# Optimization experiments

Hardware: AMD Instinct MI355X
Metric: run time of the kernel (lower is better)

Reference implementation:

```python
import jax, jax.numpy as jnp
import numpy as np

NUM_HEADS = 8


def setup_inputs() -> dict:
    key = jax.random.key(0)
    ks = jax.random.split(key, 10)
    B, S, E = 2, 2048, 1024
    return {
        "X": jax.random.normal(ks[0], (B, S, E), dtype=jnp.float32),
        "residual_score": jax.random.normal(ks[1], (S, S), dtype=jnp.float32) * 0.02,
        "Wq": jax.random.normal(ks[2], (E, E), dtype=jnp.float32) * 0.02,
        "Wk": jax.random.normal(ks[3], (E, E), dtype=jnp.float32) * 0.02,
        "Wv": jax.random.normal(ks[4], (E, E), dtype=jnp.float32) * 0.02,
        "Wepi": jax.random.normal(ks[5], (S, S), dtype=jnp.float32) * 0.02,
        "bq": jax.random.normal(ks[6], (S, 1), dtype=jnp.float32) * 0.02,
        "bk": jax.random.normal(ks[7], (S, 1), dtype=jnp.float32) * 0.02,
        "bv": jax.random.normal(ks[8], (S, 1), dtype=jnp.float32) * 0.02,
        "bo": jax.random.normal(ks[9], (S, 1), dtype=jnp.float32) * 0.02,
    }


def _split_heads(x, H):
    # (B, S, E) -> (B*H, S, E//H)
    B, S, E = x.shape
    return x.reshape(B, S, H, E // H).transpose(0, 2, 1, 3).reshape(B * H, S, E // H)


def _merge_heads(x, H):
    # (B*H, S, hd) -> (B, S, hd*H)
    BH, S, hd = x.shape
    B = BH // H
    return x.reshape(B, H, S, hd).transpose(0, 2, 1, 3).reshape(B, S, hd * H)


def reference(X, residual_score, Wq, Wk, Wv, Wepi, bq, bk, bv, bo):
    B, S, E = X.shape
    H = NUM_HEADS
    # QKV projections; biases are (S,1) broadcast over the feature axis
    q = X @ Wq + bq
    k = X @ Wk + bk
    v = X @ Wv + bv
    q = _split_heads(q, H)  # (B*H, S, hd)
    k = _split_heads(k, H)
    v = _split_heads(v, H)
    # NOTE: scaled by sqrt(seq_length), as in the original module
    attn = jnp.einsum('bsd,btd->bst', q, k) / jnp.sqrt(jnp.float32(S))
    attn = attn + residual_score  # (S,S) broadcasts over B*H
    score = jax.nn.softmax(attn, axis=-1) * Wepi  # learned elementwise mask
    effect = jnp.einsum('bst,btd->bsd', score, v)  # (B*H, S, hd)
    effect = _merge_heads(effect, H) + bo  # (B, S, E)
    return (effect, attn)
```

## Files before the change

kernel.cpp:

```cpp
#include <hip/hip_runtime.h>
#include <hip/hip_bf16.h>
#include <stdint.h>

#define S_LEN 2048
#define E_DIM 1024
#define NHEAD 8
#define HDIM 128
#define SCALE 0.022097086912079608f

typedef __attribute__((ext_vector_type(8))) short short8;
typedef __attribute__((ext_vector_type(4))) float f32x4;

__device__ __forceinline__ ushort f2bf(float f) {
  __hip_bfloat16 h = __float2bfloat16(f);
  return __builtin_bit_cast(ushort, h);
}

__device__ __forceinline__ void gload_lds16(const void* g, void* l) {
  __builtin_amdgcn_global_load_lds(
      (const __attribute__((address_space(1))) uint32_t*)g,
      (__attribute__((address_space(3))) uint32_t*)l, 16, 0, 0);
}

__global__ void cast_x_kernel(const float* __restrict__ X, ushort* __restrict__ Xb) {
  int i = (blockIdx.x * 256 + threadIdx.x) * 4;
  float4 v = *(const float4*)(X + i);
  ushort4 o;
  o.x = f2bf(v.x); o.y = f2bf(v.y); o.z = f2bf(v.z); o.w = f2bf(v.w);
  *(ushort4*)(Xb + i) = o;
}

__global__ void transpose_w_kernel(const float* __restrict__ W0, const float* __restrict__ W1,
                                   const float* __restrict__ W2, ushort* __restrict__ WT) {
  const float* W = blockIdx.z == 0 ? W0 : (blockIdx.z == 1 ? W1 : W2);
  ushort* out = WT + (size_t)blockIdx.z * E_DIM * E_DIM;
  int tk = blockIdx.x * 64, tn = blockIdx.y * 64;
  __shared__ float t[64][65];
  int tid = threadIdx.x;
  int rbase = tid >> 4;
  int cc4 = (tid & 15) * 4;
#pragma unroll
  for (int q = 0; q < 4; q++) {
    int row = q * 16 + rbase;
    float4 v = *(const float4*)(W + (size_t)(tk + row) * E_DIM + tn + cc4);
    t[row][cc4] = v.x; t[row][cc4 + 1] = v.y; t[row][cc4 + 2] = v.z; t[row][cc4 + 3] = v.w;
  }
  __syncthreads();
#pragma unroll
  for (int q = 0; q < 4; q++) {
    int row = q * 16 + rbase;
    ushort4 o;
    o.x = f2bf(t[cc4 + 0][row]);
    o.y = f2bf(t[cc4 + 1][row]);
    o.z = f2bf(t[cc4 + 2][row]);
    o.w = f2bf(t[cc4 + 3][row]);
    *(ushort4*)(out + (size_t)(tn + row) * E_DIM + tk + cc4) = o;
  }
}

__global__ __launch_bounds__(256)
void qkv_gemm_kernel(const ushort* __restrict__ Xb, const ushort* __restrict__ WT,
                     const float* __restrict__ bq, const float* __restrict__ bk,
                     const float* __restrict__ bv,
                     ushort* __restrict__ Qb, ushort* __restrict__ Kb, ushort* __restrict__ Vt) {
  int p = blockIdx.z;
  const ushort* Wp = WT + (size_t)p * E_DIM * E_DIM;
  const float* bias = (p == 0) ? bq : ((p == 1) ? bk : bv);
  int tm = blockIdx.x, tn = blockIdx.y;
  __shared__ ushort lA[128 * 64];
  __shared__ ushort lB[128 * 64];
  int tid = threadIdx.x, lane = tid & 63, w = tid >> 6;
  int wr = (w >> 1) * 64, wc = (w & 1) * 64;
  f32x4 acc[4][4] = {};
  const char* gA = (const char*)(Xb + (size_t)(tm * 128) * E_DIM);
  const char* gB = (const char*)(Wp + (size_t)(tn * 128) * E_DIM);
  char* sA = (char*)lA;
  char* sB = (char*)lB;
  for (int ks = 0; ks < E_DIM / 64; ks++) {
    int k0 = ks * 64;
#pragma unroll
    for (int rr = 0; rr < 4; rr++) {
      int c = rr * 256 + tid;
      int row = c >> 3, cc = c & 7;
      int sc = cc ^ (row & 7);
      size_t goff = ((size_t)row * E_DIM + k0 + sc * 8) * 2;
      int loff = (rr * 256 + (w << 6)) * 16;
      gload_lds16(gA + goff, sA + loff);
      gload_lds16(gB + goff, sB + loff);
    }
    __syncthreads();
#pragma unroll
    for (int kk = 0; kk < 2; kk++) {
      short8 af[4], bfr[4];
#pragma unroll
      for (int m = 0; m < 4; m++) {
        int row = wr + m * 16 + (lane & 15);
        int ch = (kk * 4 + (lane >> 4)) ^ (row & 7);
        af[m] = *(const short8*)(sA + row * 128 + ch * 16);
      }
#pragma unroll
      for (int n = 0; n < 4; n++) {
        int row = wc + n * 16 + (lane & 15);
        int ch = (kk * 4 + (lane >> 4)) ^ (row & 7);
        bfr[n] = *(const short8*)(sB + row * 128 + ch * 16);
      }
#pragma unroll
      for (int m = 0; m < 4; m++)
#pragma unroll
        for (int n = 0; n < 4; n++)
          acc[m][n] = __builtin_amdgcn_mfma_f32_16x16x32_bf16(af[m], bfr[n], acc[m][n], 0, 0, 0);
    }
    __syncthreads();
  }
#pragma unroll
  for (int m = 0; m < 4; m++) {
#pragma unroll
    for (int ri = 0; ri < 4; ri++) {
      int rg = tm * 128 + wr + m * 16 + (lane >> 4) * 4 + ri;
      float bsv = bias[rg & (S_LEN - 1)];
#pragma unroll
      for (int n = 0; n < 4; n++) {
        int cg = tn * 128 + wc + n * 16 + (lane & 15);
        ushort o = f2bf(acc[m][n][ri] + bsv);
        if (p == 0) {
          Qb[(size_t)rg * E_DIM + cg] = o;
        } else if (p == 1) {
          Kb[(size_t)rg * E_DIM + cg] = o;
        } else {
          int bb = rg >> 11, s2 = rg & (S_LEN - 1), hh = cg >> 7, dd = cg & (HDIM - 1);
          Vt[(((size_t)(bb * NHEAD + hh)) * HDIM + dd) * S_LEN + s2] = o;
        }
      }
    }
  }
}

__global__ __launch_bounds__(256)
void attn_gemm_kernel(const ushort* __restrict__ Qb, const ushort* __restrict__ Kb,
                      const float* __restrict__ resid, float* __restrict__ attn_out) {
  int tm = blockIdx.x, tn = blockIdx.y, bh = blockIdx.z;
  int b = bh >> 3, h = bh & 7;
  __shared__ ushort lA[128 * 64];
  __shared__ ushort lB[128 * 64];
  int tid = threadIdx.x, lane = tid & 63, w = tid >> 6;
  int wr = (w >> 1) * 64, wc = (w & 1) * 64;
  f32x4 acc[4][4] = {};
  const char* gA = (const char*)(Qb + ((size_t)(b * S_LEN + tm * 128)) * E_DIM + h * HDIM);
  const char* gB = (const char*)(Kb + ((size_t)(b * S_LEN + tn * 128)) * E_DIM + h * HDIM);
  char* sA = (char*)lA;
  char* sB = (char*)lB;
  for (int ks = 0; ks < 2; ks++) {
    int k0 = ks * 64;
#pragma unroll
    for (int rr = 0; rr < 4; rr++) {
      int c = rr * 256 + tid;
      int row = c >> 3, cc = c & 7;
      int sc = cc ^ (row & 7);
      size_t goff = ((size_t)row * E_DIM + k0 + sc * 8) * 2;
      int loff = (rr * 256 + (w << 6)) * 16;
      gload_lds16(gA + goff, sA + loff);
      gload_lds16(gB + goff, sB + loff);
    }
    __syncthreads();
#pragma unroll
    for (int kk = 0; kk < 2; kk++) {
      short8 af[4], bfr[4];
#pragma unroll
      for (int m = 0; m < 4; m++) {
        int row = wr + m * 16 + (lane & 15);
        int ch = (kk * 4 + (lane >> 4)) ^ (row & 7);
        af[m] = *(const short8*)(sA + row * 128 + ch * 16);
      }
#pragma unroll
      for (int n = 0; n < 4; n++) {
        int row = wc + n * 16 + (lane & 15);
        int ch = (kk * 4 + (lane >> 4)) ^ (row & 7);
        bfr[n] = *(const short8*)(sB + row * 128 + ch * 16);
      }
#pragma unroll
      for (int m = 0; m < 4; m++)
#pragma unroll
        for (int n = 0; n < 4; n++)
          acc[m][n] = __builtin_amdgcn_mfma_f32_16x16x32_bf16(af[m], bfr[n], acc[m][n], 0, 0, 0);
    }
    __syncthreads();
  }
  float* outp = attn_out + (size_t)bh * S_LEN * S_LEN;
#pragma unroll
  for (int m = 0; m < 4; m++) {
#pragma unroll
    for (int ri = 0; ri < 4; ri++) {
      int sg = tm * 128 + wr + m * 16 + (lane >> 4) * 4 + ri;
#pragma unroll
      for (int n = 0; n < 4; n++) {
        int tg = tn * 128 + wc + n * 16 + (lane & 15);
        outp[(size_t)sg * S_LEN + tg] = acc[m][n][ri] * SCALE + resid[(size_t)sg * S_LEN + tg];
      }
    }
  }
}

__global__ __launch_bounds__(256)
void pv_gemm_kernel(const float* __restrict__ attn, const float* __restrict__ Wepi,
                    const ushort* __restrict__ Vt, const float* __restrict__ bo,
                    float* __restrict__ effect) {
  int tm = blockIdx.x, bh = blockIdx.y;
  int b = bh >> 3, h = bh & 7;
  __shared__ ushort lA[128 * 64];
  __shared__ ushort lB[128 * 64];
  __shared__ float l_lds[256];
  int tid = threadIdx.x, lane = tid & 63, w = tid >> 6;
  int wr = (w >> 1) * 64, wc = (w & 1) * 64;
  f32x4 acc[4][4] = {};
  float lsum = 0.f;
  int r = tid >> 1, half = tid & 1;
  const float* aRow = attn + (size_t)bh * S_LEN * S_LEN + (size_t)(tm * 128 + r) * S_LEN + half * 32;
  const float* wRow = Wepi + (size_t)(tm * 128 + r) * S_LEN + half * 32;
  const char* gB = (const char*)(Vt + (size_t)bh * HDIM * S_LEN);
  char* sA = (char*)lA;
  char* sB = (char*)lB;
  for (int ks = 0; ks < S_LEN / 64; ks++) {
    int t0 = ks * 64;
#pragma unroll
    for (int rr = 0; rr < 4; rr++) {
      int c = rr * 256 + tid;
      int row = c >> 3, cc = c & 7;
      int sc = cc ^ (row & 7);
      gload_lds16(gB + ((size_t)row * S_LEN + t0 + sc * 8) * 2, sB + (rr * 256 + (w << 6)) * 16);
    }
#pragma unroll
    for (int cgrp = 0; cgrp < 4; cgrp++) {
      float4 a0 = *(const float4*)(aRow + t0 + cgrp * 8);
      float4 a1 = *(const float4*)(aRow + t0 + cgrp * 8 + 4);
      float4 w0 = *(const float4*)(wRow + t0 + cgrp * 8);
      float4 w1 = *(const float4*)(wRow + t0 + cgrp * 8 + 4);
      float e0 = __expf(a0.x), e1 = __expf(a0.y), e2 = __expf(a0.z), e3 = __expf(a0.w);
      float e4 = __expf(a1.x), e5 = __expf(a1.y), e6 = __expf(a1.z), e7 = __expf(a1.w);
      lsum += (e0 + e1 + e2 + e3) + (e4 + e5 + e6 + e7);
      short8 pk;
      pk[0] = (short)f2bf(e0 * w0.x); pk[1] = (short)f2bf(e1 * w0.y);
      pk[2] = (short)f2bf(e2 * w0.z); pk[3] = (short)f2bf(e3 * w0.w);
      pk[4] = (short)f2bf(e4 * w1.x); pk[5] = (short)f2bf(e5 * w1.y);
      pk[6] = (short)f2bf(e6 * w1.z); pk[7] = (short)f2bf(e7 * w1.w);
      int ch = (half * 4 + cgrp) ^ (r & 7);
      *(short8*)(sA + r * 128 + ch * 16) = pk;
    }
    __syncthreads();
#pragma unroll
    for (int kk = 0; kk < 2; kk++) {
      short8 af[4], bfr[4];
#pragma unroll
      for (int m = 0; m < 4; m++) {
        int row = wr + m * 16 + (lane & 15);
        int ch = (kk * 4 + (lane >> 4)) ^ (row & 7);
        af[m] = *(const short8*)(sA + row * 128 + ch * 16);
      }
#pragma unroll
      for (int n = 0; n < 4; n++) {
        int row = wc + n * 16 + (lane & 15);
        int ch = (kk * 4 + (lane >> 4)) ^ (row & 7);
        bfr[n] = *(const short8*)(sB + row * 128 + ch * 16);
      }
#pragma unroll
      for (int m = 0; m < 4; m++)
#pragma unroll
        for (int n = 0; n < 4; n++)
          acc[m][n] = __builtin_amdgcn_mfma_f32_16x16x32_bf16(af[m], bfr[n], acc[m][n], 0, 0, 0);
    }
    __syncthreads();
  }
  l_lds[tid] = lsum;
  __syncthreads();
#pragma unroll
  for (int m = 0; m < 4; m++) {
#pragma unroll
    for (int ri = 0; ri < 4; ri++) {
      int rl = wr + m * 16 + (lane >> 4) * 4 + ri;
      int sg = tm * 128 + rl;
      float linv = 1.0f / (l_lds[2 * rl] + l_lds[2 * rl + 1]);
      float bov = bo[sg];
#pragma unroll
      for (int n = 0; n < 4; n++) {
        int dg = wc + n * 16 + (lane & 15);
        effect[((size_t)(b * S_LEN + sg)) * E_DIM + h * HDIM + dg] = acc[m][n][ri] * linv + bov;
      }
    }
  }
}

extern "C" void kernel_launch(void* const* d_in, const int* in_sizes, int n_in,
                              void* d_out, int out_size, void* d_ws, size_t ws_size,
                              hipStream_t stream) {
  const float* X    = (const float*)d_in[0];
  const float* resd = (const float*)d_in[1];
  const float* Wq   = (const float*)d_in[2];
  const float* Wk   = (const float*)d_in[3];
  const float* Wv   = (const float*)d_in[4];
  const float* Wepi = (const float*)d_in[5];
  const float* bq   = (const float*)d_in[6];
  const float* bk   = (const float*)d_in[7];
  const float* bv   = (const float*)d_in[8];
  const float* bo   = (const float*)d_in[9];

  float* effect = (float*)d_out;
  float* attn   = (float*)d_out + (size_t)2 * S_LEN * E_DIM;

  char* ws = (char*)d_ws;
  ushort* Xb = (ushort*)(ws);
  ushort* WT = (ushort*)(ws + 8388608);
  ushort* Qb = (ushort*)(ws + 14680064);
  ushort* Kb = (ushort*)(ws + 23068672);
  ushort* Vt = (ushort*)(ws + 31457280);

  hipLaunchKernelGGL(cast_x_kernel, dim3(4096), dim3(256), 0, stream, X, Xb);
  hipLaunchKernelGGL(transpose_w_kernel, dim3(16, 16, 3), dim3(256), 0, stream, Wq, Wk, Wv, WT);
  hipLaunchKernelGGL(qkv_gemm_kernel, dim3(32, 8, 3), dim3(256), 0, stream,
                     Xb, WT, bq, bk, bv, Qb, Kb, Vt);
  hipLaunchKernelGGL(attn_gemm_kernel, dim3(16, 16, 16), dim3(256), 0, stream,
                     Qb, Kb, resd, attn);
  hipLaunchKernelGGL(pv_gemm_kernel, dim3(16, 16), dim3(256), 0, stream,
                     attn, Wepi, Vt, bo, effect);
}
```

Baseline: 554.4 us.

## Fuse exp and Wepi masking into attn epilogue, emit bf16 P and partial row sums

The exp, Wepi multiply and row-sum partials move into the QK^T kernel's epilogue, which writes a bf16 P matrix and per-tile row sums to workspace. The PV kernel then streams bf16 P with async global-to-LDS loads instead of re-reading the fp32 attention output and Wepi. Its tile shrinks to 64 rows so the grid doubles to 512 blocks for better occupancy. In exchange there is an extra bf16 write of P (about 134MB) plus Wepi reads in the first kernel, while fp32 re-reads in the PV kernel are removed.

```diff
diff --git a/kernel.cpp b/kernel.cpp
--- a/kernel.cpp
+++ b/kernel.cpp
@@ -137,11 +137,14 @@
 
 __global__ __launch_bounds__(256)
 void attn_gemm_kernel(const ushort* __restrict__ Qb, const ushort* __restrict__ Kb,
-                      const float* __restrict__ resid, float* __restrict__ attn_out) {
+                      const float* __restrict__ resid, const float* __restrict__ Wepi,
+                      float* __restrict__ attn_out, ushort* __restrict__ P,
+                      float* __restrict__ rsum) {
   int tm = blockIdx.x, tn = blockIdx.y, bh = blockIdx.z;
   int b = bh >> 3, h = bh & 7;
   __shared__ ushort lA[128 * 64];
   __shared__ ushort lB[128 * 64];
+  __shared__ float rs_lds[128][2];
   int tid = threadIdx.x, lane = tid & 63, w = tid >> 6;
   int wr = (w >> 1) * 64, wc = (w & 1) * 64;
   f32x4 acc[4][4] = {};
@@ -186,71 +189,83 @@
     __syncthreads();
   }
   float* outp = attn_out + (size_t)bh * S_LEN * S_LEN;
+  ushort* Pp = P + (size_t)bh * S_LEN * S_LEN;
 #pragma unroll
   for (int m = 0; m < 4; m++) {
 #pragma unroll
     for (int ri = 0; ri < 4; ri++) {
-      int sg = tm * 128 + wr + m * 16 + (lane >> 4) * 4 + ri;
+      int rl = wr + m * 16 + (lane >> 4) * 4 + ri;
+      int sg = tm * 128 + rl;
+      float psum = 0.f;
 #pragma unroll
       for (int n = 0; n < 4; n++) {
         int tg = tn * 128 + wc + n * 16 + (lane & 15);
-        outp[(size_t)sg * S_LEN + tg] = acc[m][n][ri] * SCALE + resid[(size_t)sg * S_LEN + tg];
-      }
-    }
+        size_t idx = (size_t)sg * S_LEN + tg;
+        float av = acc[m][n][ri] * SCALE + resid[idx];
+        outp[idx] = av;
+        float e = __expf(av);
+        psum += e;
+        Pp[idx] = f2bf(e * Wepi[idx]);
+      }
+      psum += __shfl_xor(psum, 1);
+      psum += __shfl_xor(psum, 2);
+      psum += __shfl_xor(psum, 4);
+      psum += __shfl_xor(psum, 8);
+      if ((lane & 15) == 0) rs_lds[rl][w & 1] = psum;
+    }
+  }
+  __syncthreads();
+  if (tid < 128) {
+    float s = rs_lds[tid][0] + rs_lds[tid][1];
+    rsum[((size_t)bh * S_LEN + tm * 128 + tid) * 16 + tn] = s;
   }
 }
 
 __global__ __launch_bounds__(256)
-void pv_gemm_kernel(const float* __restrict__ attn, const float* __restrict__ Wepi,
-                    const ushort* __restrict__ Vt, const float* __restrict__ bo,
+void pv_gemm_kernel(const ushort* __restrict__ P, const ushort* __restrict__ Vt,
+                    const float* __restrict__ rsum, const float* __restrict__ bo,
                     float* __restrict__ effect) {
   int tm = blockIdx.x, bh = blockIdx.y;
   int b = bh >> 3, h = bh & 7;
-  __shared__ ushort lA[128 * 64];
+  __shared__ ushort lA[64 * 64];
   __shared__ ushort lB[128 * 64];
-  __shared__ float l_lds[256];
+  __shared__ float linv_lds[64];
   int tid = threadIdx.x, lane = tid & 63, w = tid >> 6;
-  int wr = (w >> 1) * 64, wc = (w & 1) * 64;
-  f32x4 acc[4][4] = {};
-  float lsum = 0.f;
-  int r = tid >> 1, half = tid & 1;
-  const float* aRow = attn + (size_t)bh * S_LEN * S_LEN + (size_t)(tm * 128 + r) * S_LEN + half * 32;
-  const float* wRow = Wepi + (size_t)(tm * 128 + r) * S_LEN + half * 32;
+  int wr = (w >> 1) * 32, wc = (w & 1) * 64;
+  f32x4 acc[2][4] = {};
+  if (tid < 64) {
+    const float* rp = rsum + ((size_t)bh * S_LEN + tm * 64 + tid) * 16;
+    float s = 0.f;
+#pragma unroll
+    for (int j = 0; j < 16; j++) s += rp[j];
+    linv_lds[tid] = 1.0f / s;
+  }
+  const char* gA = (const char*)(P + (size_t)bh * S_LEN * S_LEN + (size_t)(tm * 64) * S_LEN);
   const char* gB = (const char*)(Vt + (size_t)bh * HDIM * S_LEN);
   char* sA = (char*)lA;
   char* sB = (char*)lB;
   for (int ks = 0; ks < S_LEN / 64; ks++) {
     int t0 = ks * 64;
 #pragma unroll
+    for (int rr = 0; rr < 2; rr++) {
+      int c = rr * 256 + tid;
+      int row = c >> 3, cc = c & 7;
+      int sc = cc ^ (row & 7);
+      gload_lds16(gA + ((size_t)row * S_LEN + t0 + sc * 8) * 2, sA + (rr * 256 + (w << 6)) * 16);
+    }
+#pragma unroll
     for (int rr = 0; rr < 4; rr++) {
       int c = rr * 256 + tid;
       int row = c >> 3, cc = c & 7;
       int sc = cc ^ (row & 7);
       gload_lds16(gB + ((size_t)row * S_LEN + t0 + sc * 8) * 2, sB + (rr * 256 + (w << 6)) * 16);
     }
-#pragma unroll
-    for (int cgrp = 0; cgrp < 4; cgrp++) {
-      float4 a0 = *(const float4*)(aRow + t0 + cgrp * 8);
-      float4 a1 = *(const float4*)(aRow + t0 + cgrp * 8 + 4);
-      float4 w0 = *(const float4*)(wRow + t0 + cgrp * 8);
-      float4 w1 = *(const float4*)(wRow + t0 + cgrp * 8 + 4);
-      float e0 = __expf(a0.x), e1 = __expf(a0.y), e2 = __expf(a0.z), e3 = __expf(a0.w);
-      float e4 = __expf(a1.x), e5 = __expf(a1.y), e6 = __expf(a1.z), e7 = __expf(a1.w);
-      lsum += (e0 + e1 + e2 + e3) + (e4 + e5 + e6 + e7);
-      short8 pk;
-      pk[0] = (short)f2bf(e0 * w0.x); pk[1] = (short)f2bf(e1 * w0.y);
-      pk[2] = (short)f2bf(e2 * w0.z); pk[3] = (short)f2bf(e3 * w0.w);
-      pk[4] = (short)f2bf(e4 * w1.x); pk[5] = (short)f2bf(e5 * w1.y);
-      pk[6] = (short)f2bf(e6 * w1.z); pk[7] = (short)f2bf(e7 * w1.w);
-      int ch = (half * 4 + cgrp) ^ (r & 7);
-      *(short8*)(sA + r * 128 + ch * 16) = pk;
-    }
     __syncthreads();
 #pragma unroll
     for (int kk = 0; kk < 2; kk++) {
-      short8 af[4], bfr[4];
-#pragma unroll
-      for (int m = 0; m < 4; m++) {
+      short8 af[2], bfr[4];
+#pragma unroll
+      for (int m = 0; m < 2; m++) {
         int row = wr + m * 16 + (lane & 15);
         int ch = (kk * 4 + (lane >> 4)) ^ (row & 7);
         af[m] = *(const short8*)(sA + row * 128 + ch * 16);
@@ -262,22 +277,20 @@
         bfr[n] = *(const short8*)(sB + row * 128 + ch * 16);
       }
 #pragma unroll
-      for (int m = 0; m < 4; m++)
+      for (int m = 0; m < 2; m++)
 #pragma unroll
         for (int n = 0; n < 4; n++)
           acc[m][n] = __builtin_amdgcn_mfma_f32_16x16x32_bf16(af[m], bfr[n], acc[m][n], 0, 0, 0);
     }
     __syncthreads();
   }
-  l_lds[tid] = lsum;
-  __syncthreads();
-#pragma unroll
-  for (int m = 0; m < 4; m++) {
+#pragma unroll
+  for (int m = 0; m < 2; m++) {
 #pragma unroll
     for (int ri = 0; ri < 4; ri++) {
       int rl = wr + m * 16 + (lane >> 4) * 4 + ri;
-      int sg = tm * 128 + rl;
-      float linv = 1.0f / (l_lds[2 * rl] + l_lds[2 * rl + 1]);
+      int sg = tm * 64 + rl;
+      float linv = linv_lds[rl];
       float bov = bo[sg];
 #pragma unroll
       for (int n = 0; n < 4; n++) {
@@ -306,18 +319,20 @@
   float* attn   = (float*)d_out + (size_t)2 * S_LEN * E_DIM;
 
   char* ws = (char*)d_ws;
-  ushort* Xb = (ushort*)(ws);
-  ushort* WT = (ushort*)(ws + 8388608);
-  ushort* Qb = (ushort*)(ws + 14680064);
-  ushort* Kb = (ushort*)(ws + 23068672);
-  ushort* Vt = (ushort*)(ws + 31457280);
+  ushort* Xb   = (ushort*)(ws);
+  ushort* WT   = (ushort*)(ws + 8388608);
+  ushort* Qb   = (ushort*)(ws + 14680064);
+  ushort* Kb   = (ushort*)(ws + 23068672);
+  ushort* Vt   = (ushort*)(ws + 31457280);
+  ushort* P    = (ushort*)(ws + 39845888);
+  float*  rsum = (float*)(ws + 174063616);
 
   hipLaunchKernelGGL(cast_x_kernel, dim3(4096), dim3(256), 0, stream, X, Xb);
   hipLaunchKernelGGL(transpose_w_kernel, dim3(16, 16, 3), dim3(256), 0, stream, Wq, Wk, Wv, WT);
   hipLaunchKernelGGL(qkv_gemm_kernel, dim3(32, 8, 3), dim3(256), 0, stream,
                      Xb, WT, bq, bk, bv, Qb, Kb, Vt);
   hipLaunchKernelGGL(attn_gemm_kernel, dim3(16, 16, 16), dim3(256), 0, stream,
-                     Qb, Kb, resd, attn);
-  hipLaunchKernelGGL(pv_gemm_kernel, dim3(16, 16), dim3(256), 0, stream,
-                     attn, Wepi, Vt, bo, effect);
-}
+                     Qb, Kb, resd, Wepi, attn, P, rsum);
+  hipLaunchKernelGGL(pv_gemm_kernel, dim3(32, 16), dim3(256), 0, stream,
+                     P, Vt, rsum, bo, effect);
+}
```

Result: faster. 541.7 us (-2.3%).
